# Kernel optimization log

Measured on AMD Instinct MI355X. Metric: run time of the kernel, lower is better.

## Reference

```python
import jax, jax.numpy as jnp
import numpy as np

N, M, E = 20000, 2000, 320000
D_MODEL, HID, HEADS = 128, 128, 4
EPS_BN = 1e-5


def _seg_softmax(a, seg, n):
    # torch_geometric.utils.softmax grouped by seg (here: destination node)
    m = jax.ops.segment_max(a, seg, num_segments=n)
    e = jnp.exp(a - m[seg])
    s = jax.ops.segment_sum(e, seg, num_segments=n)
    return e / (s[seg] + 1e-16)


def _bn(x, g, b):
    # BatchNorm1d, training-mode batch statistics (biased var), affine
    mu = x.mean(0)
    v = x.var(0)
    return (x - mu) * jax.lax.rsqrt(v + EPS_BN) * g + b


def _hconv(x, attr, node_idx, edge_idx, w_edge, lin_w, att, bias, heads):
    # PyG HypergraphConv(use_attention=True, concat=False), dropout off (eval)
    nN, nM = x.shape[0], w_edge.shape[0]
    C = lin_w.shape[1] // heads
    xh = (x @ lin_w).reshape(nN, heads, C)      # node feats per head
    ah = (attr @ lin_w).reshape(nM, heads, C)   # hyperedge feats per head
    x_i = xh[node_idx]                          # [E,H,C] gather per incidence
    a_j = ah[edge_idx]                          # [E,H,C]
    alpha = (x_i * att[:, :C]).sum(-1) + (a_j * att[:, C:]).sum(-1)  # [E,H]
    alpha = jax.nn.leaky_relu(alpha, 0.2)
    alpha = _seg_softmax(alpha, node_idx, nN)
    # D = sum of incident hyperedge weights per node; B = 1/edge_degree * w
    Dd = jax.ops.segment_sum(w_edge[edge_idx], node_idx, num_segments=nN)
    Dinv = jnp.where(Dd > 0, 1.0 / Dd, 0.0)
    Bd = jax.ops.segment_sum(jnp.ones((node_idx.shape[0],), x.dtype), edge_idx, num_segments=nM)
    Binv = jnp.where(Bd > 0, 1.0 / Bd, 0.0) * w_edge
    # node -> hyperedge
    m1 = Binv[edge_idx][:, None, None] * alpha[:, :, None] * x_i
    out_e = jax.ops.segment_sum(m1, edge_idx, num_segments=nM)  # [M,H,C]
    # hyperedge -> node
    m2 = Dinv[node_idx][:, None, None] * alpha[:, :, None] * out_e[edge_idx]
    out_n = jax.ops.segment_sum(m2, node_idx, num_segments=nN)  # [N,H,C]
    return out_n.mean(axis=1) + bias            # concat=False -> head mean


def _forward(x, node_idx, edge_idx, hyperedge_weight, W1, b1, g1, be1,
             lin_w1, att1, bias1, g2, be2, lin_w2, att2, bias2, g3, be3,
             W2, b2, g4, be4):
    nM = hyperedge_weight.shape[0]
    src = x
    h = jax.nn.leaky_relu(x @ W1 + b1, 0.2)
    h = _bn(h, g1, be1)
    # hyperedge_attr = (a.T @ x) == segment_sum of node feats per hyperedge
    attr = jax.ops.segment_sum(h[node_idx], edge_idx, num_segments=nM)
    h = _bn(h + _hconv(h, attr, node_idx, edge_idx, hyperedge_weight,
                       lin_w1, att1, bias1, HEADS), g2, be2)
    attr = jax.ops.segment_sum(h[node_idx], edge_idx, num_segments=nM)
    h = _bn(h + _hconv(h, attr, node_idx, edge_idx, hyperedge_weight,
                       lin_w2, att2, bias2, 1), g3, be3)
    o = jax.nn.leaky_relu(h @ W2 + b2, 0.2)
    return _bn(src + o, g4, be4)


def setup_inputs() -> dict:
    key = jax.random.key(0)
    ks = jax.random.split(key, 12)
    s1 = 1.0 / np.sqrt(D_MODEL)
    s2 = 1.0 / np.sqrt(HID)
    return {
        "x": jax.random.normal(ks[0], (N, D_MODEL), jnp.float32),
        "node_idx": jax.random.randint(ks[1], (E,), 0, N),
        "edge_idx": jax.random.randint(ks[2], (E,), 0, M),
        "hyperedge_weight": jax.random.uniform(ks[3], (M,), jnp.float32, 0.5, 1.5),
        "W1": jax.random.normal(ks[4], (D_MODEL, HID), jnp.float32) * s1,
        "b1": jnp.zeros((HID,), jnp.float32),
        "g1": jnp.ones((HID,), jnp.float32),
        "be1": jnp.zeros((HID,), jnp.float32),
        "lin_w1": jax.random.normal(ks[5], (HID, HEADS * HID), jnp.float32) * s2,
        "att1": jax.random.normal(ks[6], (HEADS, 2 * HID), jnp.float32) * s2,
        "bias1": jnp.zeros((HID,), jnp.float32),
        "g2": jnp.ones((HID,), jnp.float32),
        "be2": jnp.zeros((HID,), jnp.float32),
        "lin_w2": jax.random.normal(ks[7], (HID, HID), jnp.float32) * s2,
        "att2": jax.random.normal(ks[8], (1, 2 * HID), jnp.float32) * s2,
        "bias2": jnp.zeros((HID,), jnp.float32),
        "g3": jnp.ones((HID,), jnp.float32),
        "be3": jnp.zeros((HID,), jnp.float32),
        "W2": jax.random.normal(ks[9], (HID, D_MODEL), jnp.float32) * s2,
        "b2": jnp.zeros((D_MODEL,), jnp.float32),
        "g4": jnp.ones((D_MODEL,), jnp.float32),
        "be4": jnp.zeros((D_MODEL,), jnp.float32),
    }


def reference(x, node_idx, edge_idx, hyperedge_weight, W1, b1, g1, be1,
              lin_w1, att1, bias1, g2, be2, lin_w2, att2, bias2, g3, be3,
              W2, b2, g4, be4):
    return _forward(x, node_idx, edge_idx, hyperedge_weight, W1, b1, g1, be1,
                    lin_w1, att1, bias1, g2, be2, lin_w2, att2, bias2,
                    g3, be3, W2, b2, g4, be4)
```

## Files before the change

### kernel.cpp

```cpp
#include <hip/hip_runtime.h>

#define NN 20000
#define MM 2000
#define EE 320000
#define NSLICE 8
static constexpr float SLOPE = 0.2f;
static constexpr float EPSBN = 1e-5f;

__device__ inline float4 f4add(float4 a, float4 b) {
  return make_float4(a.x + b.x, a.y + b.y, a.z + b.z, a.w + b.w);
}
__device__ inline float4 f4fma(float a, float4 v, float4 c) {
  return make_float4(c.x + a * v.x, c.y + a * v.y, c.z + a * v.z, c.w + a * v.w);
}
__device__ inline float leaky(float v) { return (v > 0.f) ? v : SLOPE * v; }

__device__ inline void bn_sc4(const float* __restrict__ st, const float* __restrict__ g,
                              const float* __restrict__ be, float ninv, int c4,
                              float4& sc, float4& sh) {
  float* scp = &sc.x;
  float* shp = &sh.x;
#pragma unroll
  for (int j = 0; j < 4; j++) {
    int c = c4 * 4 + j;
    float mu = st[c] * ninv;
    float var = st[128 + c] * ninv - mu * mu;
    float s = g[c] * rsqrtf(var + EPSBN);
    scp[j] = s;
    shp[j] = be[c] - mu * s;
  }
}

__global__ void k_count(const int* __restrict__ ni, const int* __restrict__ ei,
                        int* cntN, int* cntE, int* __restrict__ rank_n,
                        int* __restrict__ rank_e) {
  int e = blockIdx.x * 256 + threadIdx.x;
  if (e >= EE) return;
  int s = blockIdx.x & (NSLICE - 1);
  rank_n[e] = atomicAdd(&cntN[s * NN + ni[e]], 1);
  rank_e[e] = atomicAdd(&cntE[s * MM + ei[e]], 1);
}

__global__ void k_slicescan(int* __restrict__ cntN, int* __restrict__ totN,
                            int* __restrict__ cntE, int* __restrict__ totE) {
  int i = blockIdx.x * 256 + threadIdx.x;
  if (i < NN) {
    int run = 0;
#pragma unroll
    for (int s = 0; s < NSLICE; s++) {
      int t = cntN[s * NN + i];
      cntN[s * NN + i] = run;
      run += t;
    }
    totN[i] = run;
  } else if (i < NN + MM) {
    int m = i - NN;
    int run = 0;
#pragma unroll
    for (int s = 0; s < NSLICE; s++) {
      int t = cntE[s * MM + m];
      cntE[s * MM + m] = run;
      run += t;
    }
    totE[m] = run;
  }
}

__global__ __launch_bounds__(1024) void k_scan2(const int* __restrict__ cntA,
                                                int* __restrict__ offA, int nA,
                                                const int* __restrict__ cntB,
                                                int* __restrict__ offB, int nB) {
  const int* cnt = blockIdx.x ? cntB : cntA;
  int* off = blockIdx.x ? offB : offA;
  int n = blockIdx.x ? nB : nA;
  __shared__ int swav[16];
  __shared__ int sCarry;
  int t = threadIdx.x;
  int lane = t & 63, wid = t >> 6;
  if (t == 0) sCarry = 0;
  __syncthreads();
  for (int base = 0; base < n; base += 1024) {
    int i = base + t;
    int v = (i < n) ? cnt[i] : 0;
    int x = v;
#pragma unroll
    for (int o = 1; o < 64; o <<= 1) {
      int y = __shfl_up(x, o);
      if (lane >= o) x += y;
    }
    if (lane == 63) swav[wid] = x;
    __syncthreads();
    if (wid == 0) {
      int s = (lane < 16) ? swav[lane] : 0;
#pragma unroll
      for (int o = 1; o < 16; o <<= 1) {
        int y = __shfl_up(s, o);
        if (lane >= o) s += y;
      }
      if (lane < 16) swav[lane] = s;
    }
    __syncthreads();
    int wpre = wid ? swav[wid - 1] : 0;
    int total = swav[15];
    if (i < n) off[i] = sCarry + wpre + x - v;
    __syncthreads();
    if (t == 0) sCarry += total;
    __syncthreads();
  }
  if (t == 0) off[n] = sCarry;
}

__global__ void k_fill(const int* __restrict__ ni, const int* __restrict__ ei,
                       const int* __restrict__ noff, const int* __restrict__ eoff,
                       const int* __restrict__ cntN, const int* __restrict__ cntE,
                       const int* __restrict__ rank_n, const int* __restrict__ rank_e,
                       int* __restrict__ em_n, int2* __restrict__ npos_e) {
  int e = blockIdx.x * 256 + threadIdx.x;
  if (e >= EE) return;
  int s = blockIdx.x & (NSLICE - 1);
  int n = ni[e];
  int m = ei[e];
  int pn = noff[n] + cntN[s * NN + n] + rank_n[e];
  int pe = eoff[m] + cntE[s * MM + m] + rank_e[e];
  em_n[pn] = m;
  npos_e[pe] = make_int2(n, pn);
}

__global__ __launch_bounds__(256) void k_gemm128(
    const float* __restrict__ A, const float* __restrict__ W,
    const float* __restrict__ bias, const float* __restrict__ resid,
    const float* __restrict__ st, const float* __restrict__ g,
    const float* __restrict__ be, float ninv, float* __restrict__ out,
    float* __restrict__ stout, int rows) {
  __shared__ float As[32][68];
  __shared__ float Ws[32][132];
  __shared__ float scs[128], shs[128];
  if (st && threadIdx.x < 128) {
    int c = threadIdx.x;
    float mu = st[c] * ninv;
    float var = st[128 + c] * ninv - mu * mu;
    float s = g[c] * rsqrtf(var + EPSBN);
    scs[c] = s;
    shs[c] = be[c] - mu * s;
  }
  if (st) __syncthreads();
  int tx = threadIdx.x & 15, ty = threadIdx.x >> 4;
  int r0 = blockIdx.x * 64;
  float4 acc[4][2];
#pragma unroll
  for (int j = 0; j < 4; j++) acc[j][0] = acc[j][1] = make_float4(0.f, 0.f, 0.f, 0.f);

  for (int k0 = 0; k0 < 128; k0 += 32) {
    __syncthreads();
    {
      int row = threadIdx.x >> 2, kq = threadIdx.x & 3;
      int rr = r0 + row;
      float4 a0 = make_float4(0.f, 0.f, 0.f, 0.f), a1 = a0;
      if (rr < rows) {
        const float* ap = A + (size_t)rr * 128 + k0 + kq * 8;
        a0 = ((const float4*)ap)[0];
        a1 = ((const float4*)ap)[1];
      }
      int kb = k0 + kq * 8;
      if (st) {
        a0.x = a0.x * scs[kb + 0] + shs[kb + 0];
        a0.y = a0.y * scs[kb + 1] + shs[kb + 1];
        a0.z = a0.z * scs[kb + 2] + shs[kb + 2];
        a0.w = a0.w * scs[kb + 3] + shs[kb + 3];
        a1.x = a1.x * scs[kb + 4] + shs[kb + 4];
        a1.y = a1.y * scs[kb + 5] + shs[kb + 5];
        a1.z = a1.z * scs[kb + 6] + shs[kb + 6];
        a1.w = a1.w * scs[kb + 7] + shs[kb + 7];
      }
      int kl = kq * 8;
      As[kl + 0][row] = a0.x;
      As[kl + 1][row] = a0.y;
      As[kl + 2][row] = a0.z;
      As[kl + 3][row] = a0.w;
      As[kl + 4][row] = a1.x;
      As[kl + 5][row] = a1.y;
      As[kl + 6][row] = a1.z;
      As[kl + 7][row] = a1.w;
    }
    {
      int kk = threadIdx.x >> 3, cq = threadIdx.x & 7;
      const float* wp = W + (size_t)(k0 + kk) * 128 + cq * 16;
#pragma unroll
      for (int f = 0; f < 4; f++)
        *(float4*)&Ws[kk][cq * 16 + f * 4] = ((const float4*)wp)[f];
    }
    __syncthreads();
#pragma unroll
    for (int kk = 0; kk < 32; kk++) {
      float4 a = *(const float4*)&As[kk][ty * 4];
      float4 w0 = *(const float4*)&Ws[kk][tx * 8];
      float4 w1 = *(const float4*)&Ws[kk][tx * 8 + 4];
      acc[0][0] = f4fma(a.x, w0, acc[0][0]);
      acc[0][1] = f4fma(a.x, w1, acc[0][1]);
      acc[1][0] = f4fma(a.y, w0, acc[1][0]);
      acc[1][1] = f4fma(a.y, w1, acc[1][1]);
      acc[2][0] = f4fma(a.z, w0, acc[2][0]);
      acc[2][1] = f4fma(a.z, w1, acc[2][1]);
      acc[3][0] = f4fma(a.w, w0, acc[3][0]);
      acc[3][1] = f4fma(a.w, w1, acc[3][1]);
    }
  }
  float4 b0 = ((const float4*)bias)[tx * 2];
  float4 b1 = ((const float4*)bias)[tx * 2 + 1];
  float4 cs0 = make_float4(0.f, 0.f, 0.f, 0.f), cs1 = cs0, cq0 = cs0, cq1 = cs0;
#pragma unroll
  for (int j = 0; j < 4; j++) {
    int r = r0 + ty * 4 + j;
    if (r < rows) {
      float4 o0 = acc[j][0], o1 = acc[j][1];
      o0 = make_float4(leaky(o0.x + b0.x), leaky(o0.y + b0.y), leaky(o0.z + b0.z),
                       leaky(o0.w + b0.w));
      o1 = make_float4(leaky(o1.x + b1.x), leaky(o1.y + b1.y), leaky(o1.z + b1.z),
                       leaky(o1.w + b1.w));
      if (resid) {
        float4 r0v = ((const float4*)resid)[(size_t)r * 32 + tx * 2];
        float4 r1v = ((const float4*)resid)[(size_t)r * 32 + tx * 2 + 1];
        o0 = f4add(o0, r0v);
        o1 = f4add(o1, r1v);
      }
      ((float4*)out)[(size_t)r * 32 + tx * 2] = o0;
      ((float4*)out)[(size_t)r * 32 + tx * 2 + 1] = o1;
      cs0 = f4add(cs0, o0);
      cs1 = f4add(cs1, o1);
      cq0 = make_float4(cq0.x + o0.x * o0.x, cq0.y + o0.y * o0.y, cq0.z + o0.z * o0.z,
                        cq0.w + o0.w * o0.w);
      cq1 = make_float4(cq1.x + o1.x * o1.x, cq1.y + o1.y * o1.y, cq1.z + o1.z * o1.z,
                        cq1.w + o1.w * o1.w);
    }
  }
  __syncthreads();
  float* sumb = &As[0][0];
  float* sqb = &Ws[0][0];
  *(float4*)&sumb[ty * 128 + tx * 8] = cs0;
  *(float4*)&sumb[ty * 128 + tx * 8 + 4] = cs1;
  *(float4*)&sqb[ty * 128 + tx * 8] = cq0;
  *(float4*)&sqb[ty * 128 + tx * 8 + 4] = cq1;
  __syncthreads();
  if (threadIdx.x < 128) {
    float S = 0.f, Q = 0.f;
#pragma unroll
    for (int w = 0; w < 16; w++) {
      S += sumb[w * 128 + threadIdx.x];
      Q += sqb[w * 128 + threadIdx.x];
    }
    atomicAdd(&stout[threadIdx.x], S);
    atomicAdd(&stout[128 + threadIdx.x], Q);
  }
}

template <int H>
__global__ __launch_bounds__(256) void k_oute64(const float* __restrict__ T,
                                                const float* __restrict__ linw,
                                                const int* __restrict__ eoff,
                                                const float* __restrict__ wedge,
                                                float* __restrict__ oute) {
  int h = blockIdx.y;
  __shared__ float As[32][68];
  __shared__ float Ws[32][132];
  int tx = threadIdx.x & 15, ty = threadIdx.x >> 4;
  int r0 = blockIdx.x * 64;
  const float* A = T + (size_t)h * MM * 128;
  float4 acc[4][2];
#pragma unroll
  for (int j = 0; j < 4; j++) acc[j][0] = acc[j][1] = make_float4(0.f, 0.f, 0.f, 0.f);

  for (int k0 = 0; k0 < 128; k0 += 32) {
    __syncthreads();
    {
      int row = threadIdx.x >> 2, kq = threadIdx.x & 3;
      int rr = r0 + row;
      float4 a0 = make_float4(0.f, 0.f, 0.f, 0.f), a1 = a0;
      if (rr < MM) {
        const float* ap = A + (size_t)rr * 128 + k0 + kq * 8;
        a0 = ((const float4*)ap)[0];
        a1 = ((const float4*)ap)[1];
      }
      int kb = kq * 8;
      As[kb + 0][row] = a0.x;
      As[kb + 1][row] = a0.y;
      As[kb + 2][row] = a0.z;
      As[kb + 3][row] = a0.w;
      As[kb + 4][row] = a1.x;
      As[kb + 5][row] = a1.y;
      As[kb + 6][row] = a1.z;
      As[kb + 7][row] = a1.w;
    }
    {
      int kk = threadIdx.x >> 3, cq = threadIdx.x & 7;
      const float* wp = linw + (size_t)(k0 + kk) * (128 * H) + h * 128 + cq * 16;
#pragma unroll
      for (int f = 0; f < 4; f++)
        *(float4*)&Ws[kk][cq * 16 + f * 4] = ((const float4*)wp)[f];
    }
    __syncthreads();
#pragma unroll
    for (int kk = 0; kk < 32; kk++) {
      float4 a = *(const float4*)&As[kk][ty * 4];
      float4 w0 = *(const float4*)&Ws[kk][tx * 8];
      float4 w1 = *(const float4*)&Ws[kk][tx * 8 + 4];
      acc[0][0] = f4fma(a.x, w0, acc[0][0]);
      acc[0][1] = f4fma(a.x, w1, acc[0][1]);
      acc[1][0] = f4fma(a.y, w0, acc[1][0]);
      acc[1][1] = f4fma(a.y, w1, acc[1][1]);
      acc[2][0] = f4fma(a.z, w0, acc[2][0]);
      acc[2][1] = f4fma(a.z, w1, acc[2][1]);
      acc[3][0] = f4fma(a.w, w0, acc[3][0]);
      acc[3][1] = f4fma(a.w, w1, acc[3][1]);
    }
  }
#pragma unroll
  for (int j = 0; j < 4; j++) {
    int m = r0 + ty * 4 + j;
    if (m >= MM) break;
    int d = eoff[m + 1] - eoff[m];
    float bv = (d > 0) ? wedge[m] / (float)d : 0.f;
    float4 o0 = acc[j][0], o1 = acc[j][1];
    o0 = make_float4(bv * o0.x, bv * o0.y, bv * o0.z, bv * o0.w);
    o1 = make_float4(bv * o1.x, bv * o1.y, bv * o1.z, bv * o1.w);
    ((float4*)oute)[((size_t)m * H + h) * 32 + tx * 2] = o0;
    ((float4*)oute)[((size_t)m * H + h) * 32 + tx * 2 + 1] = o1;
  }
}

__global__ __launch_bounds__(256) void k_colstats(const float4* __restrict__ X4,
                                                  int rows, float* __restrict__ st) {
  int c4 = threadIdx.x & 31, rs = threadIdx.x >> 5, wid = threadIdx.x >> 6;
  int r0 = blockIdx.x * 256;
  int rend = min(r0 + 256, rows);
  float4 s = make_float4(0.f, 0.f, 0.f, 0.f), q = s;
  for (int r = r0 + rs; r < rend; r += 8) {
    float4 v = X4[(size_t)r * 32 + c4];
    s = f4add(s, v);
    q = make_float4(q.x + v.x * v.x, q.y + v.y * v.y, q.z + v.z * v.z, q.w + v.w * v.w);
  }
  s.x += __shfl_xor(s.x, 32); s.y += __shfl_xor(s.y, 32);
  s.z += __shfl_xor(s.z, 32); s.w += __shfl_xor(s.w, 32);
  q.x += __shfl_xor(q.x, 32); q.y += __shfl_xor(q.y, 32);
  q.z += __shfl_xor(q.z, 32); q.w += __shfl_xor(q.w, 32);
  __shared__ float4 red[4][32][2];
  if ((threadIdx.x & 63) < 32) {
    red[wid][c4][0] = s;
    red[wid][c4][1] = q;
  }
  __syncthreads();
  if (threadIdx.x < 32) {
    float4 S = f4add(f4add(red[0][threadIdx.x][0], red[1][threadIdx.x][0]),
                     f4add(red[2][threadIdx.x][0], red[3][threadIdx.x][0]));
    float4 Q = f4add(f4add(red[0][threadIdx.x][1], red[1][threadIdx.x][1]),
                     f4add(red[2][threadIdx.x][1], red[3][threadIdx.x][1]));
    int c = threadIdx.x * 4;
    atomicAdd(&st[c + 0], S.x);
    atomicAdd(&st[c + 1], S.y);
    atomicAdd(&st[c + 2], S.z);
    atomicAdd(&st[c + 3], S.w);
    atomicAdd(&st[128 + c + 0], Q.x);
    atomicAdd(&st[128 + c + 1], Q.y);
    atomicAdd(&st[128 + c + 2], Q.z);
    atomicAdd(&st[128 + c + 3], Q.w);
  }
}

__global__ void k_bnapply_final(const float4* __restrict__ X4,
                                const float* __restrict__ st,
                                const float* __restrict__ g,
                                const float* __restrict__ be, float ninv,
                                float4* __restrict__ Y4, int total4) {
  int i = blockIdx.x * 256 + threadIdx.x;
  if (i >= total4) return;
  int c4 = i & 31;
  float4 sc, sh;
  bn_sc4(st, g, be, ninv, c4, sc, sh);
  float4 v = X4[i];
  Y4[i] = make_float4(v.x * sc.x + sh.x, v.y * sc.y + sh.y, v.z * sc.z + sh.z,
                      v.w * sc.w + sh.w);
}

__global__ void k_uv_all(const float* __restrict__ linw1, const float* __restrict__ att1,
                         float* __restrict__ UVT1, const float* __restrict__ linw2,
                         const float* __restrict__ att2, float* __restrict__ UVT2) {
  if (blockIdx.x < 2) {
    constexpr int H = 4;
    int idx = blockIdx.x * 256 + threadIdx.x;
    int h = idx >> 7, k = idx & 127;
    float u = 0.f, v = 0.f;
    for (int c = 0; c < 128; c++) {
      float w = linw1[(size_t)k * (128 * H) + h * 128 + c];
      u += w * att1[h * 256 + c];
      v += w * att1[h * 256 + 128 + c];
    }
    UVT1[h * 128 + k] = u;
    UVT1[(H + h) * 128 + k] = v;
  } else {
    if (threadIdx.x >= 128) return;
    int k = threadIdx.x;
    float u = 0.f, v = 0.f;
    for (int c = 0; c < 128; c++) {
      float w = linw2[(size_t)k * 128 + c];
      u += w * att2[c];
      v += w * att2[128 + c];
    }
    UVT2[k] = u;
    UVT2[128 + k] = v;
  }
}

template <int H>
__global__ void k_dots(const float4* __restrict__ X4, int rows,
                       const float* __restrict__ UVT, const float* __restrict__ st,
                       const float* __restrict__ g, const float* __restrict__ be,
                       float ninv, float* __restrict__ dotx, float* __restrict__ hv) {
  __shared__ float4 Ut[2 * H * 32];
  __shared__ float4 scl[32], shl[32];
  if (threadIdx.x < 32) {
    float4 sc, sh;
    bn_sc4(st, g, be, ninv, threadIdx.x, sc, sh);
    scl[threadIdx.x] = sc;
    shl[threadIdx.x] = sh;
  }
  for (int i = threadIdx.x; i < 2 * H * 32; i += 256) Ut[i] = ((const float4*)UVT)[i];
  __syncthreads();
  int idx = blockIdx.x * 256 + threadIdx.x;
  if (idx >= rows * 2 * H) return;
  int n = idx / (2 * H), h2 = idx - n * (2 * H);
  const float4* xr = X4 + (size_t)n * 32;
  const float4* ur = Ut + h2 * 32;
  float s = 0.f;
#pragma unroll 8
  for (int q = 0; q < 32; q++) {
    float4 a = xr[q], b = ur[q], c = scl[q], d = shl[q];
    float ax = a.x * c.x + d.x, ay = a.y * c.y + d.y;
    float az = a.z * c.z + d.z, aw = a.w * c.w + d.w;
    s += ax * b.x + ay * b.y + az * b.z + aw * b.w;
  }
  if (h2 < H)
    dotx[n * H + h2] = s;
  else
    hv[n * H + (h2 - H)] = s;
}

template <int H>
__global__ void k_dota(const float* __restrict__ hv, const int* __restrict__ eoff,
                       const int2* __restrict__ npos_e, float* __restrict__ dota) {
  int lane = threadIdx.x & 63;
  int m = blockIdx.x * 4 + (threadIdx.x >> 6);
  int s = eoff[m], t = eoff[m + 1];
  if (H == 4) {
    float4 acc = make_float4(0.f, 0.f, 0.f, 0.f);
    const float4* hv4 = (const float4*)hv;
    for (int j = s + lane; j < t; j += 64) acc = f4add(acc, hv4[npos_e[j].x]);
#pragma unroll
    for (int o = 32; o >= 1; o >>= 1) {
      acc.x += __shfl_xor(acc.x, o);
      acc.y += __shfl_xor(acc.y, o);
      acc.z += __shfl_xor(acc.z, o);
      acc.w += __shfl_xor(acc.w, o);
    }
    if (lane == 0) ((float4*)dota)[m] = acc;
  } else {
    float acc = 0.f;
    for (int j = s + lane; j < t; j += 64) acc += hv[npos_e[j].x];
#pragma unroll
    for (int o = 32; o >= 1; o >>= 1) acc += __shfl_xor(acc, o);
    if (lane == 0) dota[m] = acc;
  }
}

template <int H>
__global__ void k_softmax(const int* __restrict__ noff, const int* __restrict__ em_n,
                          const float* __restrict__ dotx, const float* __restrict__ dota,
                          const float* __restrict__ wedge, float* __restrict__ alpha,
                          float* __restrict__ Dinv) {
  int lane = threadIdx.x & 63;
  int n = blockIdx.x * 4 + (threadIdx.x >> 6);
  int s = noff[n], t = noff[n + 1];
  int deg = t - s;
  int h = lane & (H - 1);
  float dx = dotx[n * H + h];
  if (deg <= 64) {
    int em0 = 0;
    float dd = 0.f;
    if (lane < deg) {
      em0 = em_n[s + lane];
      dd = wedge[em0];
    }
#pragma unroll
    for (int o = 32; o >= 1; o >>= 1) dd += __shfl_xor(dd, o);
    if (lane == 0) Dinv[n] = (dd > 0.f) ? 1.f / dd : 0.f;

    constexpr int KMAX = (H == 4) ? 4 : 1;
    int P = deg * H;
    float vc[KMAX];
    float mx = -3.0e38f;
#pragma unroll
    for (int k = 0; k < KMAX; k++) {
      int p = lane + 64 * k;
      int idx = (H == 4) ? (p >> 2) : p;
      int em = __shfl(em0, idx);
      float v = dx + dota[em * H + h];
      v = leaky(v);
      vc[k] = v;
      if (p < P) mx = fmaxf(mx, v);
    }
#pragma unroll
    for (int o = H; o < 64; o <<= 1) mx = fmaxf(mx, __shfl_xor(mx, o));
    float sm = 0.f;
#pragma unroll
    for (int k = 0; k < KMAX; k++) {
      int p = lane + 64 * k;
      float e = __expf(vc[k] - mx);
      vc[k] = e;
      if (p < P) sm += e;
    }
#pragma unroll
    for (int o = H; o < 64; o <<= 1) sm += __shfl_xor(sm, o);
    float inv = 1.f / (sm + 1e-16f);
#pragma unroll
    for (int k = 0; k < KMAX; k++) {
      int p = lane + 64 * k;
      if (p < P) alpha[s * H + p] = vc[k] * inv;
    }
  } else {
    float dd = 0.f;
    for (int i = s + lane; i < t; i += 64) dd += wedge[em_n[i]];
#pragma unroll
    for (int o = 32; o >= 1; o >>= 1) dd += __shfl_xor(dd, o);
    if (lane == 0) Dinv[n] = (dd > 0.f) ? 1.f / dd : 0.f;
    int P = deg * H;
    float mx = -3.0e38f;
    for (int p = lane; p < P; p += 64) {
      int i = s + ((H == 4) ? (p >> 2) : p);
      float v = leaky(dx + dota[em_n[i] * H + h]);
      mx = fmaxf(mx, v);
    }
#pragma unroll
    for (int o = H; o < 64; o <<= 1) mx = fmaxf(mx, __shfl_xor(mx, o));
    float sm = 0.f;
    for (int p = lane; p < P; p += 64) {
      int i = s + ((H == 4) ? (p >> 2) : p);
      float v = leaky(dx + dota[em_n[i] * H + h]);
      sm += __expf(v - mx);
    }
#pragma unroll
    for (int o = H; o < 64; o <<= 1) sm += __shfl_xor(sm, o);
    float inv = 1.f / (sm + 1e-16f);
    for (int p = lane; p < P; p += 64) {
      int i = s + ((H == 4) ? (p >> 2) : p);
      float v = leaky(dx + dota[em_n[i] * H + h]);
      alpha[s * H + p] = __expf(v - mx) * inv;
    }
  }
}

template <int H>
__global__ __launch_bounds__(256) void k_T(const float4* __restrict__ h4raw,
                                           const int* __restrict__ eoff,
                                           const int2* __restrict__ npos_e,
                                           const float* __restrict__ alpha,
                                           const float* __restrict__ st,
                                           const float* __restrict__ g,
                                           const float* __restrict__ be, float ninv,
                                           float4* __restrict__ T4) {
  int m = blockIdx.x;
  int slot = threadIdx.x >> 5, c = threadIdx.x & 31;
  int wv = threadIdx.x >> 6;
  int s = eoff[m], t = eoff[m + 1];
  __shared__ int sofs[256];
  __shared__ float sal[256 * H];
  __shared__ float4 red[4][H][32];
  __shared__ float4 redA[4];
  __shared__ float sAsum[4];
  float4 acc[H];
#pragma unroll
  for (int hh = 0; hh < H; hh++) acc[hh] = make_float4(0.f, 0.f, 0.f, 0.f);
  float4 asum = make_float4(0.f, 0.f, 0.f, 0.f);

  for (int c0 = s; c0 < t; c0 += 256) {
    int cnt = min(256, t - c0);
    __syncthreads();
    if (threadIdx.x < cnt) {
      int2 np = npos_e[c0 + threadIdx.x];
      sofs[threadIdx.x] = np.x * 32;
      if (H == 4) {
        float4 a4 = ((const float4*)alpha)[np.y];
        ((float4*)sal)[threadIdx.x] = a4;
        asum = f4add(asum, a4);
      } else {
        float a = alpha[np.y];
        sal[threadIdx.x] = a;
        asum.x += a;
      }
    }
    __syncthreads();
#pragma unroll 4
    for (int j = slot; j < cnt; j += 8) {
      int ofs = sofs[j];
      float4 v = h4raw[(size_t)ofs + c];
      if (H == 4) {
        float4 a4 = ((const float4*)sal)[j];
        acc[0] = f4fma(a4.x, v, acc[0]);
        acc[1 % H] = f4fma(a4.y, v, acc[1 % H]);
        acc[2 % H] = f4fma(a4.z, v, acc[2 % H]);
        acc[3 % H] = f4fma(a4.w, v, acc[3 % H]);
      } else {
        acc[0] = f4fma(sal[j], v, acc[0]);
      }
    }
  }
#pragma unroll
  for (int hh = 0; hh < H; hh++) {
    float4 a = acc[hh];
    a.x += __shfl_xor(a.x, 32); a.y += __shfl_xor(a.y, 32);
    a.z += __shfl_xor(a.z, 32); a.w += __shfl_xor(a.w, 32);
    acc[hh] = a;
  }
#pragma unroll
  for (int o = 32; o >= 1; o >>= 1) {
    asum.x += __shfl_xor(asum.x, o); asum.y += __shfl_xor(asum.y, o);
    asum.z += __shfl_xor(asum.z, o); asum.w += __shfl_xor(asum.w, o);
  }
  if ((threadIdx.x & 63) < 32) {
#pragma unroll
    for (int hh = 0; hh < H; hh++) red[wv][hh][c] = acc[hh];
  }
  if ((threadIdx.x & 63) == 0) redA[wv] = asum;
  __syncthreads();
  if (threadIdx.x == 0) {
    float4 A = f4add(f4add(redA[0], redA[1]), f4add(redA[2], redA[3]));
    sAsum[0] = A.x; sAsum[1] = A.y; sAsum[2] = A.z; sAsum[3] = A.w;
  }
  __syncthreads();
  if (threadIdx.x < 32 * H) {
    int hh = threadIdx.x >> 5, cc = threadIdx.x & 31;
    float4 r = f4add(f4add(red[0][hh][cc], red[1][hh][cc]),
                     f4add(red[2][hh][cc], red[3][hh][cc]));
    float as = sAsum[hh];
    float4 sc, sh;
    bn_sc4(st, g, be, ninv, cc, sc, sh);
    r = make_float4(sc.x * r.x + sh.x * as, sc.y * r.y + sh.y * as,
                    sc.z * r.z + sh.z * as, sc.w * r.w + sh.w * as);
    T4[((size_t)hh * MM + m) * 32 + cc] = r;
  }
}

template <int H>
__global__ __launch_bounds__(256) void k_phase9(
    const int* __restrict__ noff, const int* __restrict__ em_n,
    const float* __restrict__ alpha, const float4* __restrict__ oute4,
    const float* __restrict__ Dinv, const float* __restrict__ bias,
    const float4* __restrict__ hres4, const float* __restrict__ st,
    const float* __restrict__ g, const float* __restrict__ be, float ninv,
    float4* __restrict__ out4) {
  int wv = threadIdx.x >> 6, lane = threadIdx.x & 63;
  int n = blockIdx.x * 4 + wv;
  int slot = lane >> 5, c = lane & 31;
  int s = noff[n], t = noff[n + 1];
  int deg = t - s;
  float4 acc = make_float4(0.f, 0.f, 0.f, 0.f);
  if (deg <= 64) {
    int m_l = 0;
    float4 a_l = make_float4(0.f, 0.f, 0.f, 0.f);
    if (lane < deg) {
      m_l = em_n[s + lane];
      if (H == 4)
        a_l = ((const float4*)alpha)[s + lane];
      else
        a_l.x = alpha[s + lane];
    }
    for (int i = slot; i < deg; i += 2) {
      int m = __shfl(m_l, i);
      if (H == 4) {
        float ax = __shfl(a_l.x, i), ay = __shfl(a_l.y, i);
        float az = __shfl(a_l.z, i), aw = __shfl(a_l.w, i);
        const float4* base = oute4 + (size_t)m * 128 + c;
        acc = f4fma(ax, base[0], acc);
        acc = f4fma(ay, base[32], acc);
        acc = f4fma(az, base[64], acc);
        acc = f4fma(aw, base[96], acc);
      } else {
        float a = __shfl(a_l.x, i);
        acc = f4fma(a, oute4[(size_t)m * 32 + c], acc);
      }
    }
  } else {
    for (int i = s + slot; i < t; i += 2) {
      int m = em_n[i];
      if (H == 4) {
        float4 a4 = ((const float4*)alpha)[i];
        const float4* base = oute4 + (size_t)m * 128 + c;
        acc = f4fma(a4.x, base[0], acc);
        acc = f4fma(a4.y, base[32], acc);
        acc = f4fma(a4.z, base[64], acc);
        acc = f4fma(a4.w, base[96], acc);
      } else {
        acc = f4fma(alpha[i], oute4[(size_t)m * 32 + c], acc);
      }
    }
  }
  acc.x += __shfl_xor(acc.x, 32); acc.y += __shfl_xor(acc.y, 32);
  acc.z += __shfl_xor(acc.z, 32); acc.w += __shfl_xor(acc.w, 32);
  if (slot == 0) {
    float scn = Dinv[n] * (1.f / H);
    float4 scB, shB;
    bn_sc4(st, g, be, ninv, c, scB, shB);
    float4 hr = hres4[(size_t)n * 32 + c];
    hr = make_float4(hr.x * scB.x + shB.x, hr.y * scB.y + shB.y, hr.z * scB.z + shB.z,
                     hr.w * scB.w + shB.w);
    float4 bi = ((const float4*)bias)[c];
    out4[(size_t)n * 32 + c] =
        make_float4(hr.x + scn * acc.x + bi.x, hr.y + scn * acc.y + bi.y,
                    hr.z + scn * acc.z + bi.z, hr.w + scn * acc.w + bi.w);
  }
}

static inline size_t alignup(size_t x) { return (x + 255) & ~(size_t)255; }

extern "C" void kernel_launch(void* const* d_in, const int* in_sizes, int n_in,
                              void* d_out, int out_size, void* d_ws, size_t ws_size,
                              hipStream_t stream) {
  const float* x = (const float*)d_in[0];
  const int* node_idx = (const int*)d_in[1];
  const int* edge_idx = (const int*)d_in[2];
  const float* wedge = (const float*)d_in[3];
  const float* W1 = (const float*)d_in[4];
  const float* b1 = (const float*)d_in[5];
  const float* g1 = (const float*)d_in[6];
  const float* be1 = (const float*)d_in[7];
  const float* linw1 = (const float*)d_in[8];
  const float* att1 = (const float*)d_in[9];
  const float* bias1 = (const float*)d_in[10];
  const float* g2 = (const float*)d_in[11];
  const float* be2 = (const float*)d_in[12];
  const float* linw2 = (const float*)d_in[13];
  const float* att2 = (const float*)d_in[14];
  const float* bias2 = (const float*)d_in[15];
  const float* g3 = (const float*)d_in[16];
  const float* be3 = (const float*)d_in[17];
  const float* W2 = (const float*)d_in[18];
  const float* b2 = (const float*)d_in[19];
  const float* g4 = (const float*)d_in[20];
  const float* be4 = (const float*)d_in[21];
  float* out = (float*)d_out;

  char* ws = (char*)d_ws;
  size_t off = 0;
  auto alloc = [&](size_t bytes) -> void* {
    void* p = ws + off;
    off = alignup(off + bytes);
    return p;
  };
  float* buf0 = (float*)alloc((size_t)NN * 128 * 4);
  float* buf1 = (float*)alloc((size_t)NN * 128 * 4);
  float* Tbuf = (float*)alloc((size_t)4 * MM * 128 * 4);
  float* oute = (float*)alloc((size_t)MM * 4 * 128 * 4);
  float* alpha = (float*)alloc((size_t)EE * 4 * 4);
  float* dotx = (float*)alloc((size_t)NN * 4 * 4);
  float* hv = (float*)alloc((size_t)NN * 4 * 4);
  float* dota = (float*)alloc((size_t)MM * 4 * 4);
  float* UVT1 = (float*)alloc(128 * 8 * 4);
  float* UVT2 = (float*)alloc(128 * 2 * 4);
  float* Dinv = (float*)alloc((size_t)NN * 4);
  int* noff = (int*)alloc((size_t)(NN + 1) * 4);
  int* eoff = (int*)alloc((size_t)(MM + 1) * 4);
  int* em_n = (int*)alloc((size_t)EE * 4);
  int2* npos_e = (int2*)alloc((size_t)EE * 8);
  int* rank_n = (int*)alloc((size_t)EE * 4);
  int* rank_e = (int*)alloc((size_t)EE * 4);
  int* totN = (int*)alloc((size_t)NN * 4);
  int* totE = (int*)alloc((size_t)MM * 4);
  size_t zero_bytes = ((size_t)NSLICE * (NN + MM) + 4 * 256) * 4;
  int* zero_region = (int*)alloc(zero_bytes);
  int* cntN = zero_region;
  int* cntE = cntN + NSLICE * NN;
  float* bnst = (float*)(cntE + NSLICE * MM);
  (void)ws_size;
  (void)in_sizes;
  (void)n_in;
  (void)out_size;

  (void)hipMemsetAsync(zero_region, 0, zero_bytes, stream);

  k_uv_all<<<3, 256, 0, stream>>>(linw1, att1, UVT1, linw2, att2, UVT2);

  k_count<<<(EE + 255) / 256, 256, 0, stream>>>(node_idx, edge_idx, cntN, cntE,
                                                rank_n, rank_e);
  k_slicescan<<<(NN + MM + 255) / 256, 256, 0, stream>>>(cntN, totN, cntE, totE);
  k_scan2<<<2, 1024, 0, stream>>>(totN, noff, NN, totE, eoff, MM);
  k_fill<<<(EE + 255) / 256, 256, 0, stream>>>(node_idx, edge_idx, noff, eoff, cntN,
                                               cntE, rank_n, rank_e, em_n, npos_e);

  const float ninv = 1.f / (float)NN;
  const int gemm_grid = (NN + 63) / 64;
  const int cs_grid = (NN + 255) / 256;
  float* st0 = bnst + 0 * 256;
  float* st1 = bnst + 1 * 256;
  float* st2 = bnst + 2 * 256;
  float* st3 = bnst + 3 * 256;

  k_gemm128<<<gemm_grid, 256, 0, stream>>>(x, W1, b1, nullptr, nullptr, nullptr,
                                           nullptr, 0.f, buf0, st0, NN);

  k_dots<4><<<(NN * 8 + 255) / 256, 256, 0, stream>>>((const float4*)buf0, NN, UVT1,
                                                      st0, g1, be1, ninv, dotx, hv);
  k_dota<4><<<MM / 4, 256, 0, stream>>>(hv, eoff, npos_e, dota);
  k_softmax<4><<<NN / 4, 256, 0, stream>>>(noff, em_n, dotx, dota, wedge, alpha, Dinv);
  k_T<4><<<MM, 256, 0, stream>>>((const float4*)buf0, eoff, npos_e, alpha, st0, g1,
                                 be1, ninv, (float4*)Tbuf);
  {
    dim3 g((MM + 63) / 64, 4);
    k_oute64<4><<<g, 256, 0, stream>>>(Tbuf, linw1, eoff, wedge, oute);
  }
  k_phase9<4><<<NN / 4, 256, 0, stream>>>(noff, em_n, alpha, (const float4*)oute, Dinv,
                                          bias1, (const float4*)buf0, st0, g1, be1,
                                          ninv, (float4*)buf1);
  k_colstats<<<cs_grid, 256, 0, stream>>>((const float4*)buf1, NN, st1);

  k_dots<1><<<(NN * 2 + 255) / 256, 256, 0, stream>>>((const float4*)buf1, NN, UVT2,
                                                      st1, g2, be2, ninv, dotx, hv);
  k_dota<1><<<MM / 4, 256, 0, stream>>>(hv, eoff, npos_e, dota);
  k_softmax<1><<<NN / 4, 256, 0, stream>>>(noff, em_n, dotx, dota, wedge, alpha, Dinv);
  k_T<1><<<MM, 256, 0, stream>>>((const float4*)buf1, eoff, npos_e, alpha, st1, g2,
                                 be2, ninv, (float4*)Tbuf);
  {
    dim3 g((MM + 63) / 64, 1);
    k_oute64<1><<<g, 256, 0, stream>>>(Tbuf, linw2, eoff, wedge, oute);
  }
  k_phase9<1><<<NN / 4, 256, 0, stream>>>(noff, em_n, alpha, (const float4*)oute, Dinv,
                                          bias2, (const float4*)buf1, st1, g2, be2,
                                          ninv, (float4*)buf0);
  k_colstats<<<cs_grid, 256, 0, stream>>>((const float4*)buf0, NN, st2);

  k_gemm128<<<gemm_grid, 256, 0, stream>>>(buf0, W2, b2, x, st2, g3, be3, ninv, buf1,
                                           st3, NN);
  k_bnapply_final<<<(NN * 32 + 255) / 256, 256, 0, stream>>>(
      (const float4*)buf1, st3, g4, be4, ninv, (float4*)out, NN * 32);
}
```

Before: 315.6 us.

## Merge CSR-build kernels, slice k_fill writes, and shrink oute GEMM tile

```diff
diff --git a/kernel.cpp b/kernel.cpp
--- a/kernel.cpp
+++ b/kernel.cpp
@@ -4,6 +4,7 @@
 #define MM 2000
 #define EE 320000
 #define NSLICE 8
+#define NBC 1250
 static constexpr float SLOPE = 0.2f;
 static constexpr float EPSBN = 1e-5f;
 
@@ -31,48 +32,51 @@
   }
 }
 
-__global__ void k_count(const int* __restrict__ ni, const int* __restrict__ ei,
-                        int* cntN, int* cntE, int* __restrict__ rank_n,
-                        int* __restrict__ rank_e) {
-  int e = blockIdx.x * 256 + threadIdx.x;
-  if (e >= EE) return;
-  int s = blockIdx.x & (NSLICE - 1);
-  rank_n[e] = atomicAdd(&cntN[s * NN + ni[e]], 1);
-  rank_e[e] = atomicAdd(&cntE[s * MM + ei[e]], 1);
-}
-
-__global__ void k_slicescan(int* __restrict__ cntN, int* __restrict__ totN,
-                            int* __restrict__ cntE, int* __restrict__ totE) {
-  int i = blockIdx.x * 256 + threadIdx.x;
-  if (i < NN) {
-    int run = 0;
-#pragma unroll
-    for (int s = 0; s < NSLICE; s++) {
-      int t = cntN[s * NN + i];
-      cntN[s * NN + i] = run;
-      run += t;
-    }
-    totN[i] = run;
-  } else if (i < NN + MM) {
-    int m = i - NN;
-    int run = 0;
-#pragma unroll
-    for (int s = 0; s < NSLICE; s++) {
-      int t = cntE[s * MM + m];
-      cntE[s * MM + m] = run;
-      run += t;
-    }
-    totE[m] = run;
-  }
-}
-
-__global__ __launch_bounds__(1024) void k_scan2(const int* __restrict__ cntA,
-                                                int* __restrict__ offA, int nA,
-                                                const int* __restrict__ cntB,
-                                                int* __restrict__ offB, int nB) {
-  const int* cnt = blockIdx.x ? cntB : cntA;
-  int* off = blockIdx.x ? offB : offA;
-  int n = blockIdx.x ? nB : nA;
+__global__ void k_count_uv(const int* __restrict__ ni, const int* __restrict__ ei,
+                           int* cntN, int* cntE, int* __restrict__ rank_n,
+                           int* __restrict__ rank_e, const float* __restrict__ linw1,
+                           const float* __restrict__ att1, float* __restrict__ UVT1,
+                           const float* __restrict__ linw2,
+                           const float* __restrict__ att2, float* __restrict__ UVT2) {
+  int b = blockIdx.x;
+  if (b < NBC) {
+    int e = b * 256 + threadIdx.x;
+    int s = b & (NSLICE - 1);
+    rank_n[e] = atomicAdd(&cntN[s * NN + ni[e]], 1);
+    rank_e[e] = atomicAdd(&cntE[s * MM + ei[e]], 1);
+  } else if (b < NBC + 2) {
+    constexpr int H = 4;
+    int idx = (b - NBC) * 256 + threadIdx.x;
+    int h = idx >> 7, k = idx & 127;
+    float u = 0.f, v = 0.f;
+    for (int c = 0; c < 128; c++) {
+      float w = linw1[(size_t)k * (128 * H) + h * 128 + c];
+      u += w * att1[h * 256 + c];
+      v += w * att1[h * 256 + 128 + c];
+    }
+    UVT1[h * 128 + k] = u;
+    UVT1[(H + h) * 128 + k] = v;
+  } else {
+    if (threadIdx.x >= 128) return;
+    int k = threadIdx.x;
+    float u = 0.f, v = 0.f;
+    for (int c = 0; c < 128; c++) {
+      float w = linw2[(size_t)k * 128 + c];
+      u += w * att2[c];
+      v += w * att2[128 + c];
+    }
+    UVT2[k] = u;
+    UVT2[128 + k] = v;
+  }
+}
+
+__global__ __launch_bounds__(1024) void k_scan2(int* __restrict__ cntN,
+                                                int* __restrict__ noff,
+                                                int* __restrict__ cntE,
+                                                int* __restrict__ eoff) {
+  int* cnt = blockIdx.x ? cntE : cntN;
+  int* off = blockIdx.x ? eoff : noff;
+  int n = blockIdx.x ? MM : NN;
   __shared__ int swav[16];
   __shared__ int sCarry;
   int t = threadIdx.x;
@@ -81,7 +85,17 @@
   __syncthreads();
   for (int base = 0; base < n; base += 1024) {
     int i = base + t;
-    int v = (i < n) ? cnt[i] : 0;
+    int v = 0;
+    if (i < n) {
+      int run = 0;
+#pragma unroll
+      for (int s = 0; s < NSLICE; s++) {
+        int c = cnt[s * n + i];
+        cnt[s * n + i] = run;
+        run += c;
+      }
+      v = run;
+    }
     int x = v;
 #pragma unroll
     for (int o = 1; o < 64; o <<= 1) {
@@ -115,15 +129,17 @@
                        const int* __restrict__ cntN, const int* __restrict__ cntE,
                        const int* __restrict__ rank_n, const int* __restrict__ rank_e,
                        int* __restrict__ em_n, int2* __restrict__ npos_e) {
-  int e = blockIdx.x * 256 + threadIdx.x;
-  if (e >= EE) return;
+  int chunk = blockIdx.x >> 3;
   int s = blockIdx.x & (NSLICE - 1);
+  int e = chunk * 256 + threadIdx.x;
+  int so = chunk & (NSLICE - 1);
   int n = ni[e];
   int m = ei[e];
-  int pn = noff[n] + cntN[s * NN + n] + rank_n[e];
-  int pe = eoff[m] + cntE[s * MM + m] + rank_e[e];
-  em_n[pn] = m;
-  npos_e[pe] = make_int2(n, pn);
+  int pn = noff[n] + cntN[so * NN + n] + rank_n[e];
+  int pe = eoff[m] + cntE[so * MM + m] + rank_e[e];
+  const int SH = EE / NSLICE;
+  if (pn / SH == s) em_n[pn] = m;
+  if (pe / SH == s) npos_e[pe] = make_int2(n, pn);
 }
 
 __global__ __launch_bounds__(256) void k_gemm128(
@@ -254,41 +270,33 @@
 }
 
 template <int H>
-__global__ __launch_bounds__(256) void k_oute64(const float* __restrict__ T,
+__global__ __launch_bounds__(256) void k_oute32(const float* __restrict__ T,
                                                 const float* __restrict__ linw,
                                                 const int* __restrict__ eoff,
                                                 const float* __restrict__ wedge,
                                                 float* __restrict__ oute) {
   int h = blockIdx.y;
-  __shared__ float As[32][68];
+  __shared__ float As[32][36];
   __shared__ float Ws[32][132];
   int tx = threadIdx.x & 15, ty = threadIdx.x >> 4;
-  int r0 = blockIdx.x * 64;
+  int r0 = blockIdx.x * 32;
   const float* A = T + (size_t)h * MM * 128;
-  float4 acc[4][2];
-#pragma unroll
-  for (int j = 0; j < 4; j++) acc[j][0] = acc[j][1] = make_float4(0.f, 0.f, 0.f, 0.f);
+  float4 acc[2][2];
+#pragma unroll
+  for (int j = 0; j < 2; j++) acc[j][0] = acc[j][1] = make_float4(0.f, 0.f, 0.f, 0.f);
 
   for (int k0 = 0; k0 < 128; k0 += 32) {
     __syncthreads();
     {
-      int row = threadIdx.x >> 2, kq = threadIdx.x & 3;
+      int row = threadIdx.x >> 3, kq = threadIdx.x & 7;
       int rr = r0 + row;
-      float4 a0 = make_float4(0.f, 0.f, 0.f, 0.f), a1 = a0;
-      if (rr < MM) {
-        const float* ap = A + (size_t)rr * 128 + k0 + kq * 8;
-        a0 = ((const float4*)ap)[0];
-        a1 = ((const float4*)ap)[1];
-      }
-      int kb = kq * 8;
+      float4 a0 = make_float4(0.f, 0.f, 0.f, 0.f);
+      if (rr < MM) a0 = *(const float4*)(A + (size_t)rr * 128 + k0 + kq * 4);
+      int kb = kq * 4;
       As[kb + 0][row] = a0.x;
       As[kb + 1][row] = a0.y;
       As[kb + 2][row] = a0.z;
       As[kb + 3][row] = a0.w;
-      As[kb + 4][row] = a1.x;
-      As[kb + 5][row] = a1.y;
-      As[kb + 6][row] = a1.z;
-      As[kb + 7][row] = a1.w;
     }
     {
       int kk = threadIdx.x >> 3, cq = threadIdx.x & 7;
@@ -300,22 +308,18 @@
     __syncthreads();
 #pragma unroll
     for (int kk = 0; kk < 32; kk++) {
-      float4 a = *(const float4*)&As[kk][ty * 4];
+      float a0 = As[kk][ty * 2], a1 = As[kk][ty * 2 + 1];
       float4 w0 = *(const float4*)&Ws[kk][tx * 8];
       float4 w1 = *(const float4*)&Ws[kk][tx * 8 + 4];
-      acc[0][0] = f4fma(a.x, w0, acc[0][0]);
-      acc[0][1] = f4fma(a.x, w1, acc[0][1]);
-      acc[1][0] = f4fma(a.y, w0, acc[1][0]);
-      acc[1][1] = f4fma(a.y, w1, acc[1][1]);
-      acc[2][0] = f4fma(a.z, w0, acc[2][0]);
-      acc[2][1] = f4fma(a.z, w1, acc[2][1]);
-      acc[3][0] = f4fma(a.w, w0, acc[3][0]);
-      acc[3][1] = f4fma(a.w, w1, acc[3][1]);
-    }
-  }
-#pragma unroll
-  for (int j = 0; j < 4; j++) {
-    int m = r0 + ty * 4 + j;
+      acc[0][0] = f4fma(a0, w0, acc[0][0]);
+      acc[0][1] = f4fma(a0, w1, acc[0][1]);
+      acc[1][0] = f4fma(a1, w0, acc[1][0]);
+      acc[1][1] = f4fma(a1, w1, acc[1][1]);
+    }
+  }
+#pragma unroll
+  for (int j = 0; j < 2; j++) {
+    int m = r0 + ty * 2 + j;
     if (m >= MM) break;
     int d = eoff[m + 1] - eoff[m];
     float bv = (d > 0) ? wedge[m] / (float)d : 0.f;
@@ -378,35 +382,6 @@
   float4 v = X4[i];
   Y4[i] = make_float4(v.x * sc.x + sh.x, v.y * sc.y + sh.y, v.z * sc.z + sh.z,
                       v.w * sc.w + sh.w);
-}
-
-__global__ void k_uv_all(const float* __restrict__ linw1, const float* __restrict__ att1,
-                         float* __restrict__ UVT1, const float* __restrict__ linw2,
-                         const float* __restrict__ att2, float* __restrict__ UVT2) {
-  if (blockIdx.x < 2) {
-    constexpr int H = 4;
-    int idx = blockIdx.x * 256 + threadIdx.x;
-    int h = idx >> 7, k = idx & 127;
-    float u = 0.f, v = 0.f;
-    for (int c = 0; c < 128; c++) {
-      float w = linw1[(size_t)k * (128 * H) + h * 128 + c];
-      u += w * att1[h * 256 + c];
-      v += w * att1[h * 256 + 128 + c];
-    }
-    UVT1[h * 128 + k] = u;
-    UVT1[(H + h) * 128 + k] = v;
-  } else {
-    if (threadIdx.x >= 128) return;
-    int k = threadIdx.x;
-    float u = 0.f, v = 0.f;
-    for (int c = 0; c < 128; c++) {
-      float w = linw2[(size_t)k * 128 + c];
-      u += w * att2[c];
-      v += w * att2[128 + c];
-    }
-    UVT2[k] = u;
-    UVT2[128 + k] = v;
-  }
 }
 
 template <int H>
@@ -770,8 +745,6 @@
   int2* npos_e = (int2*)alloc((size_t)EE * 8);
   int* rank_n = (int*)alloc((size_t)EE * 4);
   int* rank_e = (int*)alloc((size_t)EE * 4);
-  int* totN = (int*)alloc((size_t)NN * 4);
-  int* totE = (int*)alloc((size_t)MM * 4);
   size_t zero_bytes = ((size_t)NSLICE * (NN + MM) + 4 * 256) * 4;
   int* zero_region = (int*)alloc(zero_bytes);
   int* cntN = zero_region;
@@ -784,18 +757,17 @@
 
   (void)hipMemsetAsync(zero_region, 0, zero_bytes, stream);
 
-  k_uv_all<<<3, 256, 0, stream>>>(linw1, att1, UVT1, linw2, att2, UVT2);
-
-  k_count<<<(EE + 255) / 256, 256, 0, stream>>>(node_idx, edge_idx, cntN, cntE,
-                                                rank_n, rank_e);
-  k_slicescan<<<(NN + MM + 255) / 256, 256, 0, stream>>>(cntN, totN, cntE, totE);
-  k_scan2<<<2, 1024, 0, stream>>>(totN, noff, NN, totE, eoff, MM);
-  k_fill<<<(EE + 255) / 256, 256, 0, stream>>>(node_idx, edge_idx, noff, eoff, cntN,
-                                               cntE, rank_n, rank_e, em_n, npos_e);
+  k_count_uv<<<NBC + 3, 256, 0, stream>>>(node_idx, edge_idx, cntN, cntE, rank_n,
+                                          rank_e, linw1, att1, UVT1, linw2, att2,
+                                          UVT2);
+  k_scan2<<<2, 1024, 0, stream>>>(cntN, noff, cntE, eoff);
+  k_fill<<<NBC * NSLICE, 256, 0, stream>>>(node_idx, edge_idx, noff, eoff, cntN, cntE,
+                                           rank_n, rank_e, em_n, npos_e);
 
   const float ninv = 1.f / (float)NN;
   const int gemm_grid = (NN + 63) / 64;
   const int cs_grid = (NN + 255) / 256;
+  const int oute_grid = (MM + 31) / 32;
   float* st0 = bnst + 0 * 256;
   float* st1 = bnst + 1 * 256;
   float* st2 = bnst + 2 * 256;
@@ -811,8 +783,8 @@
   k_T<4><<<MM, 256, 0, stream>>>((const float4*)buf0, eoff, npos_e, alpha, st0, g1,
                                  be1, ninv, (float4*)Tbuf);
   {
-    dim3 g((MM + 63) / 64, 4);
-    k_oute64<4><<<g, 256, 0, stream>>>(Tbuf, linw1, eoff, wedge, oute);
+    dim3 g(oute_grid, 4);
+    k_oute32<4><<<g, 256, 0, stream>>>(Tbuf, linw1, eoff, wedge, oute);
   }
   k_phase9<4><<<NN / 4, 256, 0, stream>>>(noff, em_n, alpha, (const float4*)oute, Dinv,
                                           bias1, (const float4*)buf0, st0, g1, be1,
@@ -826,8 +798,8 @@
   k_T<1><<<MM, 256, 0, stream>>>((const float4*)buf1, eoff, npos_e, alpha, st1, g2,
                                  be2, ninv, (float4*)Tbuf);
   {
-    dim3 g((MM + 63) / 64, 1);
-    k_oute64<1><<<g, 256, 0, stream>>>(Tbuf, linw2, eoff, wedge, oute);
+    dim3 g(oute_grid, 1);
+    k_oute32<1><<<g, 256, 0, stream>>>(Tbuf, linw2, eoff, wedge, oute);
   }
   k_phase9<1><<<NN / 4, 256, 0, stream>>>(noff, em_n, alpha, (const float4*)oute, Dinv,
                                           bias2, (const float4*)buf1, st1, g2, be2,
```

Measured after the change: 348.3 us. 10.4% more time.
